# Kernel optimization log

Measured on AMD Instinct MI355X. Metric: run time of the kernel, lower is better.

Reference implementation:

```python
import jax, jax.numpy as jnp
from jax import lax
import numpy as np

DIM, RESO, HEADS, SPLIT, B = 128, 112, 4, 7, 2
HID = 4 * DIM  # mlp_ratio=4


def _ln(x, g, b):
    m = x.mean(-1, keepdims=True)
    v = ((x - m) ** 2).mean(-1, keepdims=True)
    return (x - m) * lax.rsqrt(v + 1e-5) * g + b


def _lepe_attn(q, k, v, cw, cb, H, W, H_sp, W_sp, nh):
    # q,k,v: [B, H*W, C] (C = branch dim); cw: depthwise conv weight [C,1,3,3]
    Bq, L, C = q.shape
    hd = C // nh
    scale = hd ** -0.5
    nHw, nWw = H // H_sp, W // W_sp

    def to_win(t):  # [B,H,W,C] -> [B*nHw*nWw, nh, H_sp*W_sp, hd]
        t = t.reshape(Bq, nHw, H_sp, nWw, W_sp, C).transpose(0, 1, 3, 2, 4, 5)
        return t.reshape(-1, H_sp * W_sp, nh, hd).transpose(0, 2, 1, 3)

    qw = to_win(q.reshape(Bq, H, W, C)) * scale
    kw = to_win(k.reshape(Bq, H, W, C))

    # v path: window partition in NCHW, depthwise conv LePE per window
    vimg = v.transpose(0, 2, 1).reshape(Bq, C, H, W)
    vimg = vimg.reshape(Bq, C, nHw, H_sp, nWw, W_sp).transpose(0, 2, 4, 1, 3, 5)
    vimg = vimg.reshape(-1, C, H_sp, W_sp)  # [B', C, H_sp, W_sp]
    lepe = lax.conv_general_dilated(vimg, cw, (1, 1), 'SAME', feature_group_count=C,
                                    dimension_numbers=('NCHW', 'OIHW', 'NCHW'))
    lepe = lepe + cb[None, :, None, None]
    vw = vimg.reshape(-1, nh, hd, H_sp * W_sp).transpose(0, 1, 3, 2)
    lepe = lepe.reshape(-1, nh, hd, H_sp * W_sp).transpose(0, 1, 3, 2)

    attn = jax.nn.softmax(jnp.einsum('whnd,whmd->whnm', qw, kw), axis=-1)
    o = jnp.einsum('whnm,whmd->whnd', attn, vw) + lepe  # [B', nh, S, hd]

    # windows2img
    o = o.transpose(0, 2, 1, 3).reshape(-1, H_sp * W_sp, C)
    o = o.reshape(Bq, nHw, nWw, H_sp, W_sp, C).transpose(0, 1, 3, 2, 4, 5)
    return o.reshape(Bq, H * W, C)


def setup_inputs() -> dict:
    key = jax.random.key(0)
    ks = jax.random.split(key, 16)
    s = 0.02
    Cb = DIM // 2
    return {
        'x': jax.random.normal(ks[0], (B, RESO * RESO, DIM), jnp.float32),
        'g1': jnp.ones((DIM,), jnp.float32),
        'b1': jnp.zeros((DIM,), jnp.float32),
        'w_qkv': s * jax.random.normal(ks[1], (3 * DIM, DIM), jnp.float32),
        'conv_w0': s * jax.random.normal(ks[2], (Cb, 1, 3, 3), jnp.float32),
        'conv_b0': jnp.zeros((Cb,), jnp.float32),
        'conv_w1': s * jax.random.normal(ks[3], (Cb, 1, 3, 3), jnp.float32),
        'conv_b1': jnp.zeros((Cb,), jnp.float32),
        'w_proj': s * jax.random.normal(ks[4], (DIM, DIM), jnp.float32),
        'b_proj': jnp.zeros((DIM,), jnp.float32),
        'g2': jnp.ones((DIM,), jnp.float32),
        'b2': jnp.zeros((DIM,), jnp.float32),
        'w_fc1': s * jax.random.normal(ks[5], (HID, DIM), jnp.float32),
        'b_fc1': jnp.zeros((HID,), jnp.float32),
        'w_fc2': s * jax.random.normal(ks[6], (DIM, HID), jnp.float32),
        'b_fc2': jnp.zeros((DIM,), jnp.float32),
    }


def reference(x, g1, b1, w_qkv, conv_w0, conv_b0, conv_w1, conv_b1,
              w_proj, b_proj, g2, b2, w_fc1, b_fc1, w_fc2, b_fc2):
    Bq, L, C = x.shape
    Cb = C // 2
    nh_b = HEADS // 2
    img = _ln(x, g1, b1)
    qkv = (img @ w_qkv.T).reshape(Bq, L, 3, C)  # qkv_bias=False
    q, k, v = qkv[:, :, 0], qkv[:, :, 1], qkv[:, :, 2]
    # branch 0: horizontal stripes (H_sp=RESO, W_sp=SPLIT) on first half of channels
    x1 = _lepe_attn(q[..., :Cb], k[..., :Cb], v[..., :Cb], conv_w0, conv_b0,
                    RESO, RESO, RESO, SPLIT, nh_b)
    # branch 1: vertical stripes (H_sp=SPLIT, W_sp=RESO) on second half
    x2 = _lepe_attn(q[..., Cb:], k[..., Cb:], v[..., Cb:], conv_w1, conv_b1,
                    RESO, RESO, SPLIT, RESO, nh_b)
    att = jnp.concatenate([x1, x2], axis=2)
    att = att @ w_proj.T + b_proj
    x = x + att  # drop_path = identity (prob 0)
    y = _ln(x, g2, b2)
    h = jax.nn.gelu(y @ w_fc1.T + b_fc1, approximate=False)
    x = x + (h @ w_fc2.T + b_fc2)
    return x
```

## Files before the change

### kernel.cpp

```cpp
#include <hip/hip_runtime.h>
#include <cstdint>

#define LTOK 12544
#define BATCH 2
#define CDIM 128
#define C3 384
#define RES 112
#define NROWS (BATCH * LTOK)
#define CHUNKS 784
#define GRID 256
#define SCALE 0.17677669529663687f

#define KS_STRIDE 40
#define VT_STRIDE 800
#define KS_USHORTS (784 * KS_STRIDE)
#define VT_USHORTS (32 * VT_STRIDE)
#define PL_USHORTS (8 * 16 * 40)
#define OL_FLOATS  (8 * 16 * 36)
#define ATTN_SMEM  (2 * (KS_USHORTS + VT_USHORTS + PL_USHORTS) + 4 * OL_FLOATS)

typedef __attribute__((ext_vector_type(8))) short bf16x8;
typedef __attribute__((ext_vector_type(4))) float f32x4;

__device__ inline ushort f2b(float f) {
    union { float f; unsigned u; } v; v.f = f;
    unsigned r = (v.u + 0x7FFFu + ((v.u >> 16) & 1u)) >> 16;
    return (ushort)r;
}
__device__ inline float b2f(ushort u) {
    union { float f; unsigned u; } v; v.u = ((unsigned)u) << 16; return v.f;
}
__device__ inline float gelu_f(float a) {
    float u2 = 1.5957691216f * (a + 0.044715f * a * a * a);
    return a - a / (__expf(u2) + 1.0f);
}

__device__ inline void nij(int n, int branch, int& i, int& j) {
    if (branch == 0) { i = n / 7; j = n - i * 7; }
    else             { i = n / 112; j = n - i * 112; }
}

__global__ __launch_bounds__(256) void k_cvt(const float* __restrict__ w0, const float* __restrict__ w1,
        const float* __restrict__ w2, const float* __restrict__ w3,
        ushort* __restrict__ o0, ushort* __restrict__ o1,
        ushort* __restrict__ o2, ushort* __restrict__ o3)
{
    int idx = blockIdx.x * 256 + threadIdx.x;
    const float* src; ushort* dst; int vi;
    if      (idx < 12288) { src = w0; dst = o0; vi = idx; }
    else if (idx < 16384) { src = w1; dst = o1; vi = idx - 12288; }
    else if (idx < 32768) { src = w2; dst = o2; vi = idx - 16384; }
    else                  { src = w3; dst = o3; vi = idx - 32768; }
    float4 v = ((const float4*)src)[vi];
    ushort4 r; r.x = f2b(v.x); r.y = f2b(v.y); r.z = f2b(v.z); r.w = f2b(v.w);
    ((ushort4*)dst)[vi] = r;
}

__global__ __launch_bounds__(512) void k_ln_qkv(const float* __restrict__ x,
        const float* __restrict__ g1, const float* __restrict__ b1,
        const ushort* __restrict__ wqkv_bf, ushort* __restrict__ qkv)
{
    __shared__ ushort ys[32 * 136];
    const int tid = threadIdx.x;
    const int wv = tid >> 6, lane = tid & 63;
    const int c16 = lane & 15, g = lane >> 4;

    bf16x8 wr[3][4];
    #pragma unroll
    for (int t = 0; t < 3; ++t)
        #pragma unroll
        for (int kc = 0; kc < 4; ++kc)
            wr[t][kc] = *(const bf16x8*)&wqkv_bf[(wv * 48 + t * 16 + c16) * CDIM + kc * 32 + g * 8];

    const int r = tid >> 4, l16 = tid & 15;
    float4 gv0 = *(const float4*)(g1 + l16 * 8);
    float4 gv4 = *(const float4*)(g1 + l16 * 8 + 4);
    float4 bv0 = *(const float4*)(b1 + l16 * 8);
    float4 bv4 = *(const float4*)(b1 + l16 * 8 + 4);

    for (int c = blockIdx.x; c < CHUNKS; c += GRID) {
        const long long row0 = (long long)c * 32;

        {
            const float* xr = x + (row0 + r) * CDIM + l16 * 8;
            float4 a0 = *(const float4*)xr;
            float4 a1 = *(const float4*)(xr + 4);
            float s  = a0.x + a0.y + a0.z + a0.w + a1.x + a1.y + a1.z + a1.w;
            float s2 = a0.x*a0.x + a0.y*a0.y + a0.z*a0.z + a0.w*a0.w
                     + a1.x*a1.x + a1.y*a1.y + a1.z*a1.z + a1.w*a1.w;
            #pragma unroll
            for (int m = 8; m >= 1; m >>= 1) { s += __shfl_xor(s, m, 16); s2 += __shfl_xor(s2, m, 16); }
            const float mean = s * (1.f / 128.f);
            const float var = s2 * (1.f / 128.f) - mean * mean;
            const float rs = rsqrtf(var + 1e-5f);
            ushort4 w0, w1;
            w0.x = f2b((a0.x - mean) * rs * gv0.x + bv0.x);
            w0.y = f2b((a0.y - mean) * rs * gv0.y + bv0.y);
            w0.z = f2b((a0.z - mean) * rs * gv0.z + bv0.z);
            w0.w = f2b((a0.w - mean) * rs * gv0.w + bv0.w);
            w1.x = f2b((a1.x - mean) * rs * gv4.x + bv4.x);
            w1.y = f2b((a1.y - mean) * rs * gv4.y + bv4.y);
            w1.z = f2b((a1.z - mean) * rs * gv4.z + bv4.z);
            w1.w = f2b((a1.w - mean) * rs * gv4.w + bv4.w);
            *(ushort4*)&ys[r * 136 + l16 * 8]     = w0;
            *(ushort4*)&ys[r * 136 + l16 * 8 + 4] = w1;
        }
        __syncthreads();

        bf16x8 yb[2][4];
        #pragma unroll
        for (int mt = 0; mt < 2; ++mt)
            #pragma unroll
            for (int kc = 0; kc < 4; ++kc)
                yb[mt][kc] = *(const bf16x8*)&ys[(mt * 16 + c16) * 136 + kc * 32 + g * 8];
        __syncthreads();

        #pragma unroll
        for (int t = 0; t < 3; ++t) {
            const int n0 = wv * 48 + t * 16;
            #pragma unroll
            for (int mt = 0; mt < 2; ++mt) {
                f32x4 acc = {0.f, 0.f, 0.f, 0.f};
                #pragma unroll
                for (int kc = 0; kc < 4; ++kc)
                    acc = __builtin_amdgcn_mfma_f32_16x16x32_bf16(wr[t][kc], yb[mt][kc], acc, 0, 0, 0);
                ushort4 sv;
                sv.x = f2b(acc[0]); sv.y = f2b(acc[1]); sv.z = f2b(acc[2]); sv.w = f2b(acc[3]);
                *(ushort4*)&qkv[(row0 + mt * 16 + c16) * C3 + n0 + g * 4] = sv;
            }
        }
    }
}

__global__ __launch_bounds__(512) void k_attn2(const ushort* __restrict__ qkv,
        const float* __restrict__ cw0, const float* __restrict__ cb0,
        const float* __restrict__ cw1, const float* __restrict__ cb1,
        ushort* __restrict__ att)
{
    extern __shared__ __align__(16) char smem[];
    ushort* ks = (ushort*)smem;
    ushort* vt = ks + KS_USHORTS;
    ushort* pl = vt + VT_USHORTS;
    float*  ol = (float*)(pl + PL_USHORTS);

    const int tid = threadIdx.x;
    const int wv = tid >> 6, lane = tid & 63;
    const int g = lane >> 4, c16 = lane & 15;

    const int wh = blockIdx.x;
    const int branch = wh >> 6;
    const int idx = wh & 63;
    const int win = idx >> 1, head = idx & 1;
    const int b = win >> 4, w = win & 15;
    const int rowBase = branch ? w * 7 : 0;
    const int colBase = branch ? 0 : w * 7;
    const float* cw = branch ? cw1 : cw0;
    const float* cb = branch ? cb1 : cb0;
    const int cbase = branch * 64 + head * 32;
    const long long qkvB = (long long)b * LTOK * C3;

    if (tid < 256) {
        const int row = tid >> 3, c2 = (tid & 7) * 2;
        *(unsigned*)&vt[row * VT_STRIDE + 784 + c2] = 0u;
    }

    for (int u = tid; u < 1568; u += 512) {
        const int kp = u >> 2, d8 = (u & 3) * 8;
        const int n0 = 2 * kp;
        int i, j; nij(n0, branch, i, j);
        const long long L0 = (long long)(rowBase + i) * RES + colBase + j;
        long long L1;
        if (branch) L1 = L0 + 1;
        else        L1 = (j == 6) ? (L0 + RES - 6) : (L0 + 1);
        const ushort* p0 = qkv + qkvB + L0 * C3 + cbase + d8;
        const ushort* p1 = qkv + qkvB + L1 * C3 + cbase + d8;
        bf16x8 k0 = *(const bf16x8*)(p0 + 128);
        bf16x8 k1 = *(const bf16x8*)(p1 + 128);
        bf16x8 v0 = *(const bf16x8*)(p0 + 256);
        bf16x8 v1 = *(const bf16x8*)(p1 + 256);
        *(bf16x8*)&ks[(n0)     * KS_STRIDE + d8] = k0;
        *(bf16x8*)&ks[(n0 + 1) * KS_STRIDE + d8] = k1;
        #pragma unroll
        for (int e = 0; e < 8; ++e) {
            ushort2 pr; pr.x = (ushort)v0[e]; pr.y = (ushort)v1[e];
            *(ushort2*)&vt[(d8 + e) * VT_STRIDE + n0] = pr;
        }
    }
    __syncthreads();

    const int tbase = blockIdx.y ? 25 : 0;
    const int ntile = blockIdx.y ? 24 : 25;
    const int H_sp = branch ? 7 : RES;
    const int W_sp = branch ? RES : 7;
    ushort* pb = pl + wv * (16 * 40);
    float*  ob = ol + wv * (16 * 36);

    for (int t = wv; t < ntile; t += 8) {
        const int gt = tbase + t;
        bf16x8 qq;
        {
            int n = gt * 16 + c16;
            int i, j; nij(n, branch, i, j);
            const ushort* qp = qkv + qkvB + (long long)((rowBase + i) * RES + colBase + j) * C3 + cbase + g * 8;
            qq = *(const bf16x8*)qp;
            #pragma unroll
            for (int e = 0; e < 8; ++e) qq[e] = (short)f2b(b2f((ushort)qq[e]) * SCALE);
        }

        f32x4 O0 = {0.f,0.f,0.f,0.f}, O1 = {0.f,0.f,0.f,0.f};
        float lsum[4] = {0.f,0.f,0.f,0.f};

        for (int p = 0; p < 25; ++p) {
            bf16x8 kf0 = *(const bf16x8*)&ks[(p * 32 + c16) * KS_STRIDE + g * 8];
            bf16x8 vf0 = *(const bf16x8*)&vt[c16 * VT_STRIDE + p * 32 + g * 8];
            bf16x8 vf1 = *(const bf16x8*)&vt[(16 + c16) * VT_STRIDE + p * 32 + g * 8];
            f32x4 z = {0.f,0.f,0.f,0.f};
            f32x4 S0 = __builtin_amdgcn_mfma_f32_16x16x32_bf16(qq, kf0, z, 0, 0, 0);
            f32x4 S1 = z;
            if (p < 24) {
                bf16x8 kf1 = *(const bf16x8*)&ks[(p * 32 + 16 + c16) * KS_STRIDE + g * 8];
                S1 = __builtin_amdgcn_mfma_f32_16x16x32_bf16(qq, kf1, z, 0, 0, 0);
            }
            ushort pw0[4], pw1[4];
            #pragma unroll
            for (int r = 0; r < 4; ++r) {
                float e0 = __expf(S0[r]);
                lsum[r] += e0;
                pw0[r] = f2b(e0);
                if (p < 24) {
                    float e1 = __expf(S1[r]);
                    lsum[r] += e1;
                    pw1[r] = f2b(e1);
                } else pw1[r] = 0;
            }
            #pragma unroll
            for (int r = 0; r < 4; ++r) {
                pb[(g * 4 + r) * 40 + c16]      = pw0[r];
                pb[(g * 4 + r) * 40 + 16 + c16] = pw1[r];
            }
            bf16x8 pf = *(const bf16x8*)&pb[c16 * 40 + g * 8];
            O0 = __builtin_amdgcn_mfma_f32_16x16x32_bf16(pf, vf0, O0, 0, 0, 0);
            O1 = __builtin_amdgcn_mfma_f32_16x16x32_bf16(pf, vf1, O1, 0, 0, 0);
        }

        #pragma unroll
        for (int r = 0; r < 4; ++r) {
            float s = lsum[r];
            s += __shfl_xor(s, 1); s += __shfl_xor(s, 2);
            s += __shfl_xor(s, 4); s += __shfl_xor(s, 8);
            const float inv = 1.f / s;
            ob[(g * 4 + r) * 36 + c16]      = O0[r] * inv;
            ob[(g * 4 + r) * 36 + 16 + c16] = O1[r] * inv;
        }
        const int r2 = lane >> 2, db = (lane & 3) * 8;
        const int n0 = gt * 16 + r2;
        int i0, j0; nij(n0, branch, i0, j0);
        float acc[8];
        #pragma unroll
        for (int e = 0; e < 8; ++e) acc[e] = ob[r2 * 36 + db + e] + cb[head * 32 + db + e];
        #pragma unroll
        for (int dij = 0; dij < 9; ++dij) {
            const int di = dij / 3 - 1, dj = dij % 3 - 1;
            const int ii = i0 + di, jj = j0 + dj;
            if (ii >= 0 && ii < H_sp && jj >= 0 && jj < W_sp) {
                const ushort* vp = qkv + qkvB + (long long)((rowBase + ii) * RES + colBase + jj) * C3 + 256 + cbase + db;
                bf16x8 vv = *(const bf16x8*)vp;
                #pragma unroll
                for (int e = 0; e < 8; ++e)
                    acc[e] += cw[(head * 32 + db + e) * 9 + dij] * b2f((ushort)vv[e]);
            }
        }
        const long long Lq = (long long)(rowBase + i0) * RES + colBase + j0;
        ushort* op = att + ((long long)b * LTOK + Lq) * CDIM + cbase + db;
        bf16x8 ov;
        #pragma unroll
        for (int e = 0; e < 8; ++e) ov[e] = (short)f2b(acc[e]);
        *(bf16x8*)op = ov;
    }
}

__global__ __launch_bounds__(512) void k_pmlp(const ushort* __restrict__ att,
        const ushort* __restrict__ wproj_bf, const float* __restrict__ bproj,
        const float* __restrict__ x,
        const float* __restrict__ g2, const float* __restrict__ b2,
        const ushort* __restrict__ w1bf, const float* __restrict__ bfc1,
        const ushort* __restrict__ w2bf, const float* __restrict__ bfc2,
        float* __restrict__ out)
{
    __shared__ float  xs[32 * 132];
    __shared__ ushort ys[32 * 136];
    __shared__ ushort hs[32 * 520];
    const int tid = threadIdx.x;
    const int wv = tid >> 6, lane = tid & 63;
    const int c16 = lane & 15, g = lane >> 4;

    bf16x8 wpr[4];
    #pragma unroll
    for (int kc = 0; kc < 4; ++kc)
        wpr[kc] = *(const bf16x8*)&wproj_bf[(wv * 16 + c16) * CDIM + kc * 32 + g * 8];
    bf16x8 w1r[4][4];
    #pragma unroll
    for (int t = 0; t < 4; ++t)
        #pragma unroll
        for (int kc = 0; kc < 4; ++kc)
            w1r[t][kc] = *(const bf16x8*)&w1bf[(wv * 64 + t * 16 + c16) * CDIM + kc * 32 + g * 8];
    const float4 bpv = *(const float4*)&bproj[wv * 16 + g * 4];
    float4 b1v[4];
    #pragma unroll
    for (int t = 0; t < 4; ++t) b1v[t] = *(const float4*)&bfc1[wv * 64 + t * 16 + g * 4];
    const float4 b2v = *(const float4*)&bfc2[wv * 16 + g * 4];

    const int r = tid >> 4, l16 = tid & 15;
    float4 gv0 = *(const float4*)(g2 + l16 * 8);
    float4 gv4 = *(const float4*)(g2 + l16 * 8 + 4);
    float4 bv0 = *(const float4*)(b2 + l16 * 8);
    float4 bv4 = *(const float4*)(b2 + l16 * 8 + 4);

    for (int c = blockIdx.x; c < CHUNKS; c += GRID) {
        const long long row0 = (long long)c * 32;

        f32x4 resid[2];
        {
            bf16x8 ab[2][4];
            #pragma unroll
            for (int mt = 0; mt < 2; ++mt)
                #pragma unroll
                for (int kc = 0; kc < 4; ++kc)
                    ab[mt][kc] = *(const bf16x8*)&att[(row0 + mt * 16 + c16) * CDIM + kc * 32 + g * 8];
            const int col = wv * 16 + g * 4;
            #pragma unroll
            for (int mt = 0; mt < 2; ++mt) {
                f32x4 a = {0.f, 0.f, 0.f, 0.f};
                #pragma unroll
                for (int kc = 0; kc < 4; ++kc)
                    a = __builtin_amdgcn_mfma_f32_16x16x32_bf16(wpr[kc], ab[mt][kc], a, 0, 0, 0);
                float4 xv = *(const float4*)&x[(row0 + mt * 16 + c16) * CDIM + col];
                f32x4 rr;
                rr[0] = a[0] + xv.x + bpv.x;
                rr[1] = a[1] + xv.y + bpv.y;
                rr[2] = a[2] + xv.z + bpv.z;
                rr[3] = a[3] + xv.w + bpv.w;
                resid[mt] = rr;
                *(float4*)&xs[(mt * 16 + c16) * 132 + col] = make_float4(rr[0], rr[1], rr[2], rr[3]);
            }
        }
        __syncthreads();

        {
            float4 a0 = *(const float4*)&xs[r * 132 + l16 * 8];
            float4 a1 = *(const float4*)&xs[r * 132 + l16 * 8 + 4];
            float s  = a0.x + a0.y + a0.z + a0.w + a1.x + a1.y + a1.z + a1.w;
            float s2 = a0.x*a0.x + a0.y*a0.y + a0.z*a0.z + a0.w*a0.w
                     + a1.x*a1.x + a1.y*a1.y + a1.z*a1.z + a1.w*a1.w;
            #pragma unroll
            for (int m = 8; m >= 1; m >>= 1) { s += __shfl_xor(s, m, 16); s2 += __shfl_xor(s2, m, 16); }
            const float mean = s * (1.f / 128.f);
            const float var = s2 * (1.f / 128.f) - mean * mean;
            const float rs = rsqrtf(var + 1e-5f);
            ushort4 w0, w1;
            w0.x = f2b((a0.x - mean) * rs * gv0.x + bv0.x);
            w0.y = f2b((a0.y - mean) * rs * gv0.y + bv0.y);
            w0.z = f2b((a0.z - mean) * rs * gv0.z + bv0.z);
            w0.w = f2b((a0.w - mean) * rs * gv0.w + bv0.w);
            w1.x = f2b((a1.x - mean) * rs * gv4.x + bv4.x);
            w1.y = f2b((a1.y - mean) * rs * gv4.y + bv4.y);
            w1.z = f2b((a1.z - mean) * rs * gv4.z + bv4.z);
            w1.w = f2b((a1.w - mean) * rs * gv4.w + bv4.w);
            *(ushort4*)&ys[r * 136 + l16 * 8]     = w0;
            *(ushort4*)&ys[r * 136 + l16 * 8 + 4] = w1;
        }
        __syncthreads();

        bf16x8 yb[2][4];
        #pragma unroll
        for (int mt = 0; mt < 2; ++mt)
            #pragma unroll
            for (int kc = 0; kc < 4; ++kc)
                yb[mt][kc] = *(const bf16x8*)&ys[(mt * 16 + c16) * 136 + kc * 32 + g * 8];

        #pragma unroll
        for (int t = 0; t < 4; ++t) {
            #pragma unroll
            for (int mt = 0; mt < 2; ++mt) {
                f32x4 a = {0.f, 0.f, 0.f, 0.f};
                #pragma unroll
                for (int kc = 0; kc < 4; ++kc)
                    a = __builtin_amdgcn_mfma_f32_16x16x32_bf16(w1r[t][kc], yb[mt][kc], a, 0, 0, 0);
                ushort4 sv;
                sv.x = f2b(gelu_f(a[0] + b1v[t].x));
                sv.y = f2b(gelu_f(a[1] + b1v[t].y));
                sv.z = f2b(gelu_f(a[2] + b1v[t].z));
                sv.w = f2b(gelu_f(a[3] + b1v[t].w));
                *(ushort4*)&hs[(mt * 16 + c16) * 520 + wv * 64 + t * 16 + g * 4] = sv;
            }
        }

        bf16x8 w2r[16];
        #pragma unroll
        for (int kc = 0; kc < 16; ++kc)
            w2r[kc] = *(const bf16x8*)&w2bf[(wv * 16 + c16) * 512 + kc * 32 + g * 8];

        __syncthreads();

        f32x4 acc2[2] = {{0.f,0.f,0.f,0.f},{0.f,0.f,0.f,0.f}};
        #pragma unroll
        for (int kc = 0; kc < 16; ++kc) {
            bf16x8 hb[2];
            #pragma unroll
            for (int mt = 0; mt < 2; ++mt)
                hb[mt] = *(const bf16x8*)&hs[(mt * 16 + c16) * 520 + kc * 32 + g * 8];
            #pragma unroll
            for (int mt = 0; mt < 2; ++mt)
                acc2[mt] = __builtin_amdgcn_mfma_f32_16x16x32_bf16(w2r[kc], hb[mt], acc2[mt], 0, 0, 0);
        }

        {
            const int col = wv * 16 + g * 4;
            #pragma unroll
            for (int mt = 0; mt < 2; ++mt) {
                const long long row = row0 + mt * 16 + c16;
                float4 o;
                o.x = acc2[mt][0] + resid[mt][0] + b2v.x;
                o.y = acc2[mt][1] + resid[mt][1] + b2v.y;
                o.z = acc2[mt][2] + resid[mt][2] + b2v.z;
                o.w = acc2[mt][3] + resid[mt][3] + b2v.w;
                *(float4*)&out[row * CDIM + col] = o;
            }
        }
    }
}

extern "C" void kernel_launch(void* const* d_in, const int* in_sizes, int n_in,
                              void* d_out, int out_size, void* d_ws, size_t ws_size,
                              hipStream_t stream) {
    const float* x     = (const float*)d_in[0];
    const float* g1    = (const float*)d_in[1];
    const float* b1    = (const float*)d_in[2];
    const float* wqkv  = (const float*)d_in[3];
    const float* cw0   = (const float*)d_in[4];
    const float* cb0   = (const float*)d_in[5];
    const float* cw1   = (const float*)d_in[6];
    const float* cb1   = (const float*)d_in[7];
    const float* wproj = (const float*)d_in[8];
    const float* bproj = (const float*)d_in[9];
    const float* g2    = (const float*)d_in[10];
    const float* b2    = (const float*)d_in[11];
    const float* wfc1  = (const float*)d_in[12];
    const float* bfc1  = (const float*)d_in[13];
    const float* wfc2  = (const float*)d_in[14];
    const float* bfc2  = (const float*)d_in[15];

    char* wsb = (char*)d_ws;
    ushort* qkv_bf   = (ushort*)wsb;
    ushort* att_bf   = (ushort*)(wsb + 19267584);
    char*   wbase    = wsb + 19267584 + 6422528;
    ushort* wqkv_bf  = (ushort*)(wbase);
    ushort* wproj_bf = (ushort*)(wbase + 98304);
    ushort* wfc1_bf  = (ushort*)(wbase + 98304 + 32768);
    ushort* wfc2_bf  = (ushort*)(wbase + 98304 + 32768 + 131072);

    float* out = (float*)d_out;

    static bool attr_set = false;
    if (!attr_set) {
        hipFuncSetAttribute((const void*)k_attn2,
                            hipFuncAttributeMaxDynamicSharedMemorySize, ATTN_SMEM);
        attr_set = true;
    }

    k_cvt<<<192, 256, 0, stream>>>(wqkv, wproj, wfc1, wfc2, wqkv_bf, wproj_bf, wfc1_bf, wfc2_bf);
    k_ln_qkv<<<GRID, 512, 0, stream>>>(x, g1, b1, wqkv_bf, qkv_bf);
    k_attn2<<<dim3(128, 2), 512, ATTN_SMEM, stream>>>(qkv_bf, cw0, cb0, cw1, cb1, att_bf);
    k_pmlp<<<GRID, 512, 0, stream>>>(att_bf, wproj_bf, bproj, x, g2, b2,
                                     wfc1_bf, bfc1, wfc2_bf, bfc2, out);
}
```

Before: 111.2 us.

## Restructure stripe attention: global K prefetch, transposed scores, register-shuffle P, finer grid

The attention kernel no longer stages K in LDS. K fragments are read straight from global memory with a one-step register prefetch, and V fragments are prefetched the same way. Scores are computed transposed (K·Q), so the softmax probabilities can be packed with v_cvt_pk_bf16_f32 and rearranged through cross-lane shuffles instead of an LDS round trip. The row-sum reduction becomes two xor shuffles, and the grid is split four ways per window instead of two to raise occupancy. LDS use shrinks, but K is now re-read from global or L2 by every tile.

```diff
diff --git a/kernel.cpp b/kernel.cpp
--- a/kernel.cpp
+++ b/kernel.cpp
@@ -11,13 +11,10 @@
 #define GRID 256
 #define SCALE 0.17677669529663687f
 
-#define KS_STRIDE 40
 #define VT_STRIDE 800
-#define KS_USHORTS (784 * KS_STRIDE)
 #define VT_USHORTS (32 * VT_STRIDE)
-#define PL_USHORTS (8 * 16 * 40)
 #define OL_FLOATS  (8 * 16 * 36)
-#define ATTN_SMEM  (2 * (KS_USHORTS + VT_USHORTS + PL_USHORTS) + 4 * OL_FLOATS)
+#define ATTN_SMEM  (2 * VT_USHORTS + 4 * OL_FLOATS)
 
 typedef __attribute__((ext_vector_type(8))) short bf16x8;
 typedef __attribute__((ext_vector_type(4))) float f32x4;
@@ -132,16 +129,14 @@
     }
 }
 
-__global__ __launch_bounds__(512) void k_attn2(const ushort* __restrict__ qkv,
+__global__ __launch_bounds__(512) void k_attn3(const ushort* __restrict__ qkv,
         const float* __restrict__ cw0, const float* __restrict__ cb0,
         const float* __restrict__ cw1, const float* __restrict__ cb1,
         ushort* __restrict__ att)
 {
     extern __shared__ __align__(16) char smem[];
-    ushort* ks = (ushort*)smem;
-    ushort* vt = ks + KS_USHORTS;
-    ushort* pl = vt + VT_USHORTS;
-    float*  ol = (float*)(pl + PL_USHORTS);
+    ushort* vt = (ushort*)smem;
+    float*  ol = (float*)(vt + VT_USHORTS);
 
     const int tid = threadIdx.x;
     const int wv = tid >> 6, lane = tid & 63;
@@ -174,12 +169,8 @@
         else        L1 = (j == 6) ? (L0 + RES - 6) : (L0 + 1);
         const ushort* p0 = qkv + qkvB + L0 * C3 + cbase + d8;
         const ushort* p1 = qkv + qkvB + L1 * C3 + cbase + d8;
-        bf16x8 k0 = *(const bf16x8*)(p0 + 128);
-        bf16x8 k1 = *(const bf16x8*)(p1 + 128);
         bf16x8 v0 = *(const bf16x8*)(p0 + 256);
         bf16x8 v1 = *(const bf16x8*)(p1 + 256);
-        *(bf16x8*)&ks[(n0)     * KS_STRIDE + d8] = k0;
-        *(bf16x8*)&ks[(n0 + 1) * KS_STRIDE + d8] = k1;
         #pragma unroll
         for (int e = 0; e < 8; ++e) {
             ushort2 pr; pr.x = (ushort)v0[e]; pr.y = (ushort)v1[e];
@@ -188,12 +179,20 @@
     }
     __syncthreads();
 
-    const int tbase = blockIdx.y ? 25 : 0;
-    const int ntile = blockIdx.y ? 24 : 25;
+    const ushort* kbase = qkv + qkvB + 128 + cbase + g * 8;
+    auto tokL = [&](int n) -> int {
+        if (branch) return rowBase * RES + n;
+        int i = (n * 9363) >> 16;
+        return i * RES + colBase + (n - i * 7);
+    };
+
+    const int tbase = blockIdx.y * 12;
+    const int ntile = (blockIdx.y == 3) ? 13 : 12;
     const int H_sp = branch ? 7 : RES;
     const int W_sp = branch ? RES : 7;
-    ushort* pb = pl + wv * (16 * 40);
-    float*  ob = ol + wv * (16 * 36);
+    float* ob = ol + wv * (16 * 36);
+    const int srcA = ((g & 1) << 5) | c16;
+    const int srcB = srcA + 16;
 
     for (int t = wv; t < ntile; t += 8) {
         const int gt = tbase + t;
@@ -208,50 +207,77 @@
         }
 
         f32x4 O0 = {0.f,0.f,0.f,0.f}, O1 = {0.f,0.f,0.f,0.f};
-        float lsum[4] = {0.f,0.f,0.f,0.f};
-
+        float lsum = 0.f;
+
+        bf16x8 k0c, k1c, v0c, v1c, k0n, k1n, v0n, v1n;
+        {
+            int n = c16;
+            k0c = *(const bf16x8*)(kbase + (long long)tokL(n) * C3);
+            k1c = *(const bf16x8*)(kbase + (long long)tokL(n + 16) * C3);
+            v0c = *(const bf16x8*)&vt[c16 * VT_STRIDE + g * 8];
+            v1c = *(const bf16x8*)&vt[(16 + c16) * VT_STRIDE + g * 8];
+        }
+
+        #pragma unroll 5
         for (int p = 0; p < 25; ++p) {
-            bf16x8 kf0 = *(const bf16x8*)&ks[(p * 32 + c16) * KS_STRIDE + g * 8];
-            bf16x8 vf0 = *(const bf16x8*)&vt[c16 * VT_STRIDE + p * 32 + g * 8];
-            bf16x8 vf1 = *(const bf16x8*)&vt[(16 + c16) * VT_STRIDE + p * 32 + g * 8];
+            if (p < 24) {
+                int n = (p + 1) * 32 + c16;
+                int n1 = n + 16; if (n1 > 783) n1 = 783;
+                k0n = *(const bf16x8*)(kbase + (long long)tokL(n) * C3);
+                k1n = *(const bf16x8*)(kbase + (long long)tokL(n1) * C3);
+                v0n = *(const bf16x8*)&vt[c16 * VT_STRIDE + (p + 1) * 32 + g * 8];
+                v1n = *(const bf16x8*)&vt[(16 + c16) * VT_STRIDE + (p + 1) * 32 + g * 8];
+            }
             f32x4 z = {0.f,0.f,0.f,0.f};
-            f32x4 S0 = __builtin_amdgcn_mfma_f32_16x16x32_bf16(qq, kf0, z, 0, 0, 0);
-            f32x4 S1 = z;
+            f32x4 S0 = __builtin_amdgcn_mfma_f32_16x16x32_bf16(k0c, qq, z, 0, 0, 0);
+            float e0 = __expf(S0[0]), e1 = __expf(S0[1]);
+            float e2 = __expf(S0[2]), e3 = __expf(S0[3]);
+            float f0, f1, f2, f3;
             if (p < 24) {
-                bf16x8 kf1 = *(const bf16x8*)&ks[(p * 32 + 16 + c16) * KS_STRIDE + g * 8];
-                S1 = __builtin_amdgcn_mfma_f32_16x16x32_bf16(qq, kf1, z, 0, 0, 0);
-            }
-            ushort pw0[4], pw1[4];
-            #pragma unroll
-            for (int r = 0; r < 4; ++r) {
-                float e0 = __expf(S0[r]);
-                lsum[r] += e0;
-                pw0[r] = f2b(e0);
-                if (p < 24) {
-                    float e1 = __expf(S1[r]);
-                    lsum[r] += e1;
-                    pw1[r] = f2b(e1);
-                } else pw1[r] = 0;
-            }
-            #pragma unroll
-            for (int r = 0; r < 4; ++r) {
-                pb[(g * 4 + r) * 40 + c16]      = pw0[r];
-                pb[(g * 4 + r) * 40 + 16 + c16] = pw1[r];
-            }
-            bf16x8 pf = *(const bf16x8*)&pb[c16 * 40 + g * 8];
-            O0 = __builtin_amdgcn_mfma_f32_16x16x32_bf16(pf, vf0, O0, 0, 0, 0);
-            O1 = __builtin_amdgcn_mfma_f32_16x16x32_bf16(pf, vf1, O1, 0, 0, 0);
-        }
-
+                f32x4 S1 = __builtin_amdgcn_mfma_f32_16x16x32_bf16(k1c, qq, z, 0, 0, 0);
+                f0 = __expf(S1[0]); f1 = __expf(S1[1]);
+                f2 = __expf(S1[2]); f3 = __expf(S1[3]);
+            } else { f0 = f1 = f2 = f3 = 0.f; }
+            lsum += (e0 + e1) + (e2 + e3) + (f0 + f1) + (f2 + f3);
+
+            unsigned a0, a1, b0, b1;
+            asm("v_cvt_pk_bf16_f32 %0, %1, %2" : "=v"(a0) : "v"(e0), "v"(e1));
+            asm("v_cvt_pk_bf16_f32 %0, %1, %2" : "=v"(a1) : "v"(e2), "v"(e3));
+            asm("v_cvt_pk_bf16_f32 %0, %1, %2" : "=v"(b0) : "v"(f0), "v"(f1));
+            asm("v_cvt_pk_bf16_f32 %0, %1, %2" : "=v"(b1) : "v"(f2), "v"(f3));
+
+            int sA0 = __shfl((int)a0, srcA, 64);
+            int sA1 = __shfl((int)a1, srcA, 64);
+            int sB0 = __shfl((int)b0, srcA, 64);
+            int sB1 = __shfl((int)b1, srcA, 64);
+            int tA0 = __shfl((int)a0, srcB, 64);
+            int tA1 = __shfl((int)a1, srcB, 64);
+            int tB0 = __shfl((int)b0, srcB, 64);
+            int tB1 = __shfl((int)b1, srcB, 64);
+            const bool hi = (g >= 2);
+            int4 pi;
+            pi.x = hi ? sB0 : sA0;
+            pi.y = hi ? sB1 : sA1;
+            pi.z = hi ? tB0 : tA0;
+            pi.w = hi ? tB1 : tA1;
+            bf16x8 pf = *(bf16x8*)&pi;
+
+            O0 = __builtin_amdgcn_mfma_f32_16x16x32_bf16(pf, v0c, O0, 0, 0, 0);
+            O1 = __builtin_amdgcn_mfma_f32_16x16x32_bf16(pf, v1c, O1, 0, 0, 0);
+
+            k0c = k0n; k1c = k1n; v0c = v0n; v1c = v1n;
+        }
+
+        lsum += __shfl_xor(lsum, 16);
+        lsum += __shfl_xor(lsum, 32);
+        const float inv = 1.f / lsum;
         #pragma unroll
         for (int r = 0; r < 4; ++r) {
-            float s = lsum[r];
-            s += __shfl_xor(s, 1); s += __shfl_xor(s, 2);
-            s += __shfl_xor(s, 4); s += __shfl_xor(s, 8);
-            const float inv = 1.f / s;
-            ob[(g * 4 + r) * 36 + c16]      = O0[r] * inv;
-            ob[(g * 4 + r) * 36 + 16 + c16] = O1[r] * inv;
-        }
+            const float invr = __shfl(inv, (lane & 48) | (g * 4 + r), 64);
+            ob[(g * 4 + r) * 36 + c16]      = O0[r] * invr;
+            ob[(g * 4 + r) * 36 + 16 + c16] = O1[r] * invr;
+        }
+
         const int r2 = lane >> 2, db = (lane & 3) * 8;
         const int n0 = gt * 16 + r2;
         int i0, j0; nij(n0, branch, i0, j0);
@@ -461,16 +487,12 @@
 
     float* out = (float*)d_out;
 
-    static bool attr_set = false;
-    if (!attr_set) {
-        hipFuncSetAttribute((const void*)k_attn2,
-                            hipFuncAttributeMaxDynamicSharedMemorySize, ATTN_SMEM);
-        attr_set = true;
-    }
+    hipFuncSetAttribute((const void*)k_attn3,
+                        hipFuncAttributeMaxDynamicSharedMemorySize, ATTN_SMEM);
 
     k_cvt<<<192, 256, 0, stream>>>(wqkv, wproj, wfc1, wfc2, wqkv_bf, wproj_bf, wfc1_bf, wfc2_bf);
     k_ln_qkv<<<GRID, 512, 0, stream>>>(x, g1, b1, wqkv_bf, qkv_bf);
-    k_attn2<<<dim3(128, 2), 512, ATTN_SMEM, stream>>>(qkv_bf, cw0, cb0, cw1, cb1, att_bf);
+    k_attn3<<<dim3(128, 4), 512, ATTN_SMEM, stream>>>(qkv_bf, cw0, cb0, cw1, cb1, att_bf);
     k_pmlp<<<GRID, 512, 0, stream>>>(att_bf, wproj_bf, bproj, x, g2, b2,
                                      wfc1_bf, bfc1, wfc2_bf, bfc2, out);
 }
```

New measurement: 121.9 us. 1.1x slower.
